# Optimization experiments

Hardware: AMD Instinct MI355X
Metric: run time of the kernel (lower is better)

The kernel has to match this reference:

```python
import jax, jax.numpy as jnp
import numpy as np

B, D, H = 4096, 1024, 1024

def _glorot(key, shape):
    fan_in, fan_out = shape
    limit = np.sqrt(6.0 / (fan_in + fan_out))
    return jax.random.uniform(key, shape, jnp.float32, -limit, limit)

def setup_inputs() -> dict:
    key = jax.random.key(0)
    ks = jax.random.split(key, 12)
    inp = {
        'inputs': jax.random.normal(ks[0], (B, D), jnp.float32),
        'h_prev': jax.random.normal(ks[1], (B, H), jnp.float32),
        'c_prev': jax.random.normal(ks[2], (B, H), jnp.float32),
    }
    names = ['f', 'i', 'c', 'o']
    for j, n in enumerate(names):
        inp['W_' + n] = _glorot(ks[3 + 2 * j], (D, H))
        inp['U_' + n] = _glorot(ks[4 + 2 * j], (H, H))
        inp['b_' + n] = jnp.zeros((H,), jnp.float32)
    return inp

def reference(inputs, h_prev, c_prev, W_f, U_f, b_f, W_i, U_i, b_i, W_c, U_c, b_c, W_o, U_o, b_o):
    f_t = jax.nn.sigmoid(inputs @ W_f + h_prev @ U_f + b_f)
    i_t = jax.nn.sigmoid(inputs @ W_i + h_prev @ U_i + b_i)
    c_tilde = jnp.tanh(inputs @ W_c + h_prev @ U_c + b_c)
    c_next = f_t * c_prev + i_t * c_tilde
    o_t = jax.nn.sigmoid(inputs @ W_o + h_prev @ U_o + b_o)
    h_next = o_t * jnp.tanh(c_next)
    return (h_next, c_next)
```

## Files before the change

kernel.cpp:

```cpp
#include <hip/hip_runtime.h>


typedef __attribute__((ext_vector_type(8))) short bfrag8;
typedef __attribute__((ext_vector_type(4))) float f32x4;

__device__ __forceinline__ unsigned int f2bf(float f) {
  unsigned int u = __builtin_bit_cast(unsigned int, f);
  unsigned int r = (u + 0x7fffu + ((u >> 16) & 1u)) >> 16;
  return r & 0xffffu;
}

__global__ __launch_bounds__(256) void prep_x(const float* __restrict__ inputs,
                                              const float* __restrict__ h_prev,
                                              unsigned short* __restrict__ X) {
  int idx = blockIdx.x * 256 + threadIdx.x;
  int b  = idx >> 8;
  int k8 = (idx & 255) * 8;
  const float* src = (k8 < 1024) ? (inputs + (size_t)b * 1024 + k8)
                                 : (h_prev + (size_t)b * 1024 + (k8 - 1024));
  float4 v0 = ((const float4*)src)[0];
  float4 v1 = ((const float4*)src)[1];
  uint4 o;
  o.x = f2bf(v0.x) | (f2bf(v0.y) << 16);
  o.y = f2bf(v0.z) | (f2bf(v0.w) << 16);
  o.z = f2bf(v1.x) | (f2bf(v1.y) << 16);
  o.w = f2bf(v1.z) | (f2bf(v1.w) << 16);
  *(uint4*)(X + (size_t)b * 2048 + k8) = o;
}

__global__ __launch_bounds__(256) void prep_w(
    const float* __restrict__ s0, const float* __restrict__ s1,
    const float* __restrict__ s2, const float* __restrict__ s3,
    const float* __restrict__ s4, const float* __restrict__ s5,
    const float* __restrict__ s6, const float* __restrict__ s7,
    unsigned short* __restrict__ Wct) {
  int blk = blockIdx.x;
  int m = blk >> 8;
  const float* src = (m == 0) ? s0 : (m == 1) ? s1 : (m == 2) ? s2 : (m == 3) ? s3
                   : (m == 4) ? s4 : (m == 5) ? s5 : (m == 6) ? s6 : s7;
  int g = m >> 1, half = m & 1;
  unsigned short* dst = Wct + (size_t)g * 1024 * 2048 + (size_t)half * 1024;
  int t = blk & 255;
  int k0 = (t >> 4) * 64;
  int h0 = (t & 15) * 64;
  __shared__ float lt[64][68];
  int tid = threadIdx.x;
  #pragma unroll
  for (int it = 0; it < 4; ++it) {
    int r  = (tid >> 4) + it * 16;
    int c4 = (tid & 15) * 4;
    float4 v = *(const float4*)(src + (size_t)(k0 + r) * 1024 + h0 + c4);
    lt[r][c4 + 0] = v.x; lt[r][c4 + 1] = v.y; lt[r][c4 + 2] = v.z; lt[r][c4 + 3] = v.w;
  }
  __syncthreads();
  #pragma unroll
  for (int it = 0; it < 4; ++it) {
    int hh  = (tid >> 4) + it * 16;
    int kk4 = (tid & 15) * 4;
    uint2 o;
    o.x = f2bf(lt[kk4 + 0][hh]) | (f2bf(lt[kk4 + 1][hh]) << 16);
    o.y = f2bf(lt[kk4 + 2][hh]) | (f2bf(lt[kk4 + 3][hh]) << 16);
    *(uint2*)(dst + (size_t)(h0 + hh) * 2048 + k0 + kk4) = o;
  }
}

__global__ __launch_bounds__(256, 2) void lstm_gemm(
    const unsigned short* __restrict__ X, const unsigned short* __restrict__ Wct,
    const float* __restrict__ c_prev,
    const float* __restrict__ bfv, const float* __restrict__ biv,
    const float* __restrict__ bcv, const float* __restrict__ bov,
    float* __restrict__ out) {
  __shared__ __align__(16) char smem[49152];
  const int tid = threadIdx.x;
  const int lane = tid & 63, wid = tid >> 6;
  const int u = lane & 15, q = lane >> 4;
  const int wave_m = wid >> 1, wave_n = wid & 1;
  const int h0 = blockIdx.x * 64;
  const int row0 = blockIdx.y * 128;

  f32x4 acc[4][4][2];
  #pragma unroll
  for (int g = 0; g < 4; ++g)
    #pragma unroll
    for (int mi = 0; mi < 4; ++mi)
      #pragma unroll
      for (int ni = 0; ni < 2; ++ni)
        acc[g][mi][ni] = (f32x4){0.f, 0.f, 0.f, 0.f};

  #pragma unroll 1
  for (int kt = 0; kt < 32; ++kt) {
    const int kb = kt * 64;
    __syncthreads();
    #pragma unroll
    for (int i = 0; i < 4; ++i) {
      int c = tid + 256 * i;
      int row = c >> 3, slot = c & 7;
      int sw = slot ^ (row & 7);
      uint4 v = *(const uint4*)(X + (size_t)(row0 + row) * 2048 + kb + slot * 8);
      *(uint4*)(smem + row * 128 + sw * 16) = v;
    }
    #pragma unroll
    for (int i = 0; i < 8; ++i) {
      int c = tid + 256 * i;
      int g = c >> 9, hr = (c >> 3) & 63, slot = c & 7;
      int sw = slot ^ (hr & 7);
      uint4 v = *(const uint4*)(Wct + (size_t)((g << 10) + h0 + hr) * 2048 + kb + slot * 8);
      *(uint4*)(smem + 16384 + g * 8192 + hr * 128 + sw * 16) = v;
    }
    __syncthreads();
    #pragma unroll
    for (int kk = 0; kk < 2; ++kk) {
      bfrag8 afr[4];
      #pragma unroll
      for (int mi = 0; mi < 4; ++mi) {
        int row = wave_m * 64 + mi * 16 + u;
        int sl = (kk * 4 + q) ^ (row & 7);
        afr[mi] = *(const bfrag8*)(smem + row * 128 + sl * 16);
      }
      #pragma unroll
      for (int g = 0; g < 4; ++g) {
        #pragma unroll
        for (int ni = 0; ni < 2; ++ni) {
          int hr = wave_n * 32 + ni * 16 + u;
          int sl = (kk * 4 + q) ^ (hr & 7);
          bfrag8 bfr = *(const bfrag8*)(smem + 16384 + g * 8192 + hr * 128 + sl * 16);
          #pragma unroll
          for (int mi = 0; mi < 4; ++mi)
            acc[g][mi][ni] = __builtin_amdgcn_mfma_f32_16x16x32_bf16(
                afr[mi], bfr, acc[g][mi][ni], 0, 0, 0);
        }
      }
    }
  }

  #pragma unroll
  for (int ni = 0; ni < 2; ++ni) {
    int h = h0 + wave_n * 32 + ni * 16 + u;
    float Bf = bfv[h], Bi = biv[h], Bc = bcv[h], Bo = bov[h];
    #pragma unroll
    for (int mi = 0; mi < 4; ++mi) {
      #pragma unroll
      for (int j = 0; j < 4; ++j) {
        int b = row0 + wave_m * 64 + mi * 16 + q * 4 + j;
        float pf = acc[0][mi][ni][j] + Bf;
        float pi = acc[1][mi][ni][j] + Bi;
        float pc = acc[2][mi][ni][j] + Bc;
        float po = acc[3][mi][ni][j] + Bo;
        float fg = 1.f / (1.f + __expf(-pf));
        float ig = 1.f / (1.f + __expf(-pi));
        float ct = 2.f / (1.f + __expf(-2.f * pc)) - 1.f;
        float og = 1.f / (1.f + __expf(-po));
        float cn = fg * c_prev[(size_t)b * 1024 + h] + ig * ct;
        float hn = og * (2.f / (1.f + __expf(-2.f * cn)) - 1.f);
        out[(size_t)b * 1024 + h] = hn;
        out[(size_t)4096 * 1024 + (size_t)b * 1024 + h] = cn;
      }
    }
  }
}

extern "C" void kernel_launch(void* const* d_in, const int* in_sizes, int n_in,
                              void* d_out, int out_size, void* d_ws, size_t ws_size,
                              hipStream_t stream) {
  const float* inputs = (const float*)d_in[0];
  const float* h_prev = (const float*)d_in[1];
  const float* c_prev = (const float*)d_in[2];
  const float* Wf = (const float*)d_in[3];
  const float* Uf = (const float*)d_in[4];
  const float* bf = (const float*)d_in[5];
  const float* Wi = (const float*)d_in[6];
  const float* Ui = (const float*)d_in[7];
  const float* bi = (const float*)d_in[8];
  const float* Wc = (const float*)d_in[9];
  const float* Uc = (const float*)d_in[10];
  const float* bc = (const float*)d_in[11];
  const float* Wo = (const float*)d_in[12];
  const float* Uo = (const float*)d_in[13];
  const float* bo = (const float*)d_in[14];
  float* out = (float*)d_out;

  unsigned short* X   = (unsigned short*)d_ws;
  unsigned short* Wct = X + (size_t)4096 * 2048;

  prep_x<<<4096, 256, 0, stream>>>(inputs, h_prev, X);
  prep_w<<<2048, 256, 0, stream>>>(Wf, Uf, Wi, Ui, Wc, Uc, Wo, Uo, Wct);
  dim3 grid(16, 32);
  lstm_gemm<<<grid, 256, 0, stream>>>(X, Wct, c_prev, bf, bi, bc, bo, out);
}
```

Measured before the change: 95.61 us.

## Rewrite LSTM GEMM as 256x256-tile, 8-wave, double-buffered direct-to-LDS pipeline

Replaces the 128x64-tile GEMM with a 256-row by 64-hidden (times 4 gates) tile per 512-thread block, using 128KB of dynamic LDS. Global data is staged straight into LDS with global_load_lds, double-buffered over k and interleaved with ds_read and MFMA phases, with explicit vmcnt and lgkmcnt waits, barriers, and setprio around MFMA bursts. A block-ID swizzle is added for L2 locality. The aim is to hide global-load latency and raise reuse per LDS byte, at the cost of a much more fragile, hand-scheduled pipeline and only 256 blocks.

```diff
diff --git a/kernel.cpp b/kernel.cpp
--- a/kernel.cpp
+++ b/kernel.cpp
@@ -64,97 +64,183 @@
   }
 }
 
-__global__ __launch_bounds__(256, 2) void lstm_gemm(
+
+#define FENCE() asm volatile("" ::: "memory")
+#define BARRIER() do { FENCE(); __builtin_amdgcn_s_barrier(); FENCE(); } while (0)
+#define VMCNT(n) asm volatile("s_waitcnt vmcnt(" #n ")" ::: "memory")
+#define LGKM0_SCHED() do { asm volatile("s_waitcnt lgkmcnt(0)" ::: "memory"); \
+                           __builtin_amdgcn_sched_barrier(0); } while (0)
+#define GLOAD16(gp, lp) __builtin_amdgcn_global_load_lds( \
+    (const __attribute__((address_space(1))) unsigned int*)(gp), \
+    (__attribute__((address_space(3))) unsigned int*)(lp), 16, 0, 0)
+#define DSR(dst, addr, off) asm volatile("ds_read_b128 %0, %1 offset:%c2" \
+    : "=v"(dst) : "v"(addr), "n"(off))
+
+#define READ_A8(arr, BUF, RB) do { \
+  DSR(arr[0], aA0, (BUF)*16384 + (RB)*128 + 0);    \
+  DSR(arr[1], aA1, (BUF)*16384 + (RB)*128 + 0);    \
+  DSR(arr[2], aA0, (BUF)*16384 + (RB)*128 + 2048); \
+  DSR(arr[3], aA1, (BUF)*16384 + (RB)*128 + 2048); \
+  DSR(arr[4], aA0, (BUF)*16384 + (RB)*128 + 4096); \
+  DSR(arr[5], aA1, (BUF)*16384 + (RB)*128 + 4096); \
+  DSR(arr[6], aA0, (BUF)*16384 + (RB)*128 + 6144); \
+  DSR(arr[7], aA1, (BUF)*16384 + (RB)*128 + 6144); \
+} while (0)
+
+#define READ_B4(arr, BUF, CB) do { \
+  DSR(arr[0], aB0, (BUF)*16384 + (CB)*128 + 0);    \
+  DSR(arr[1], aB1, (BUF)*16384 + (CB)*128 + 0);    \
+  DSR(arr[2], aB0, (BUF)*16384 + (CB)*128 + 2048); \
+  DSR(arr[3], aB1, (BUF)*16384 + (CB)*128 + 2048); \
+} while (0)
+
+#define STAGE_A(BUF, H, kt) do { int _kb = ((kt) < 32 ? (kt) : 31) * 64; \
+  GLOAD16(pA0 + (size_t)(H) * 262144 + _kb, smem + (H)*32768 + (BUF)*16384 + stbase); \
+  GLOAD16(pA1 + (size_t)(H) * 262144 + _kb, smem + (H)*32768 + (BUF)*16384 + stbase + 1024); \
+} while (0)
+
+#define STAGE_B0(BUF, kt) do { int _kb = ((kt) < 32 ? (kt) : 31) * 64; \
+  GLOAD16(pB00 + _kb, smem + 65536 + (BUF)*16384 + stbase); \
+  GLOAD16(pB01 + _kb, smem + 65536 + (BUF)*16384 + stbase + 1024); \
+} while (0)
+
+#define STAGE_B1(BUF, kt) do { int _kb = ((kt) < 32 ? (kt) : 31) * 64; \
+  GLOAD16(pB10 + _kb, smem + 98304 + (BUF)*16384 + stbase); \
+  GLOAD16(pB11 + _kb, smem + 98304 + (BUF)*16384 + stbase + 1024); \
+} while (0)
+
+#define MFMA16(B4, G0, M0) do { \
+  __builtin_amdgcn_s_setprio(1); \
+  _Pragma("unroll") for (int ni = 0; ni < 2; ++ni) \
+  _Pragma("unroll") for (int mi = 0; mi < 4; ++mi) \
+  _Pragma("unroll") for (int kk = 0; kk < 2; ++kk) \
+    acc[(G0)+ni][(M0)+mi] = __builtin_amdgcn_mfma_f32_16x16x32_bf16( \
+        a[mi*2+kk], (B4)[ni*2+kk], acc[(G0)+ni][(M0)+mi], 0, 0, 0); \
+  __builtin_amdgcn_s_setprio(0); \
+} while (0)
+
+__global__ __launch_bounds__(512, 2) void lstm_gemm(
     const unsigned short* __restrict__ X, const unsigned short* __restrict__ Wct,
     const float* __restrict__ c_prev,
     const float* __restrict__ bfv, const float* __restrict__ biv,
     const float* __restrict__ bcv, const float* __restrict__ bov,
     float* __restrict__ out) {
-  __shared__ __align__(16) char smem[49152];
+  extern __shared__ __align__(16) char smem[];
   const int tid = threadIdx.x;
-  const int lane = tid & 63, wid = tid >> 6;
-  const int u = lane & 15, q = lane >> 4;
-  const int wave_m = wid >> 1, wave_n = wid & 1;
-  const int h0 = blockIdx.x * 64;
-  const int row0 = blockIdx.y * 128;
-
-  f32x4 acc[4][4][2];
+  const int lane = tid & 63, w = tid >> 6;
+  const int u = lane & 15, q = (lane >> 4) & 3;
+  const int wm = w >> 2, wn = w & 3;
+
+  const int bid = blockIdx.x;
+  const int swz = (bid & 7) * 32 + (bid >> 3);
+  const int h0 = (swz & 15) * 64;
+  const int row0 = (swz >> 4) * 256;
+
+  const unsigned lds0 = (unsigned)(size_t)((__attribute__((address_space(3))) char*)smem);
+
+  const int sw0 = (q ^ (u & 7)) << 4;
+  const int sw1 = ((q + 4) ^ (u & 7)) << 4;
+  const unsigned aA0 = lds0 + wm * 32768 + u * 128 + sw0;
+  const unsigned aA1 = lds0 + wm * 32768 + u * 128 + sw1;
+  const unsigned aB0 = lds0 + 65536 + (wn >> 1) * 32768 + ((wn & 1) * 64 + u) * 128 + sw0;
+  const unsigned aB1 = lds0 + 65536 + (wn >> 1) * 32768 + ((wn & 1) * 64 + u) * 128 + sw1;
+
+  const int stbase = w * 2048 + lane * 16;
+  const int rA0 = w * 16 + (lane >> 3), rA1 = rA0 + 8;
+  const int ssA = (lane & 7) ^ (rA0 & 7);
+  const unsigned short* pA0 = X + (size_t)(row0 + rA0) * 2048 + ssA * 8;
+  const unsigned short* pA1 = X + (size_t)(row0 + rA1) * 2048 + ssA * 8;
+  auto wrow = [&](int C) { return (((C >> 4) & 3) << 10) + h0 + ((C >> 6) << 4) + (C & 15); };
+  const unsigned short* pB00 = Wct + (size_t)wrow(rA0) * 2048 + ssA * 8;
+  const unsigned short* pB01 = Wct + (size_t)wrow(rA1) * 2048 + ssA * 8;
+  const unsigned short* pB10 = Wct + (size_t)wrow(128 + rA0) * 2048 + ssA * 8;
+  const unsigned short* pB11 = Wct + (size_t)wrow(128 + rA1) * 2048 + ssA * 8;
+
+  f32x4 acc[4][8];
   #pragma unroll
   for (int g = 0; g < 4; ++g)
     #pragma unroll
-    for (int mi = 0; mi < 4; ++mi)
-      #pragma unroll
-      for (int ni = 0; ni < 2; ++ni)
-        acc[g][mi][ni] = (f32x4){0.f, 0.f, 0.f, 0.f};
+    for (int m = 0; m < 8; ++m)
+      acc[g][m] = (f32x4){0.f, 0.f, 0.f, 0.f};
+
+  bfrag8 a[8], bh[4], bl0[4], bl1[4];
+
+  STAGE_B0(0, 0); STAGE_B1(0, 0); STAGE_A(0, 0, 0); STAGE_A(0, 1, 0);
+  STAGE_B0(1, 1); STAGE_B1(1, 1);
+  VMCNT(4);
+  BARRIER();
+  READ_B4(bl0, 0, 0);
 
   #pragma unroll 1
-  for (int kt = 0; kt < 32; ++kt) {
-    const int kb = kt * 64;
-    __syncthreads();
+  for (int t = 0; t < 16; ++t) {
+    const int kt1 = 2 * t + 1, kt2 = 2 * t + 2, kt3 = 2 * t + 3;
+    READ_A8(a, 0, 0);
+    STAGE_A(1, 0, kt1);
+    BARRIER(); LGKM0_SCHED();
+    MFMA16(bl0, 0, 0);
+    BARRIER();
+    READ_B4(bh, 0, 32);
+    STAGE_A(1, 1, kt1);
+    BARRIER(); LGKM0_SCHED();
+    MFMA16(bh, 2, 0);
+    BARRIER();
+    READ_A8(a, 0, 64);
+    STAGE_B0(0, kt2);
+    VMCNT(8);
+    BARRIER(); LGKM0_SCHED();
+    MFMA16(bh, 2, 4);
+    BARRIER();
+    READ_B4(bl1, 1, 0);
+    STAGE_B1(0, kt2);
+    VMCNT(4);
+    BARRIER(); LGKM0_SCHED();
+    MFMA16(bl0, 0, 4);
+    BARRIER();
+    READ_A8(a, 1, 0);
+    STAGE_A(0, 0, kt2);
+    BARRIER(); LGKM0_SCHED();
+    MFMA16(bl1, 0, 0);
+    BARRIER();
+    READ_B4(bh, 1, 32);
+    STAGE_A(0, 1, kt2);
+    BARRIER(); LGKM0_SCHED();
+    MFMA16(bh, 2, 0);
+    BARRIER();
+    READ_A8(a, 1, 64);
+    STAGE_B0(1, kt3);
+    VMCNT(8);
+    BARRIER(); LGKM0_SCHED();
+    MFMA16(bh, 2, 4);
+    BARRIER();
+    READ_B4(bl0, 0, 0);
+    STAGE_B1(1, kt3);
+    VMCNT(4);
+    BARRIER(); LGKM0_SCHED();
+    MFMA16(bl1, 0, 4);
+    BARRIER();
+  }
+  VMCNT(0);
+
+  const int hcol = h0 + wn * 16 + u;
+  const float Bgf = bfv[hcol], Bgi = biv[hcol], Bgc = bcv[hcol], Bgo = bov[hcol];
+  const int rbw = row0 + wm * 128;
+  #pragma unroll
+  for (int m = 0; m < 8; ++m) {
     #pragma unroll
-    for (int i = 0; i < 4; ++i) {
-      int c = tid + 256 * i;
-      int row = c >> 3, slot = c & 7;
-      int sw = slot ^ (row & 7);
-      uint4 v = *(const uint4*)(X + (size_t)(row0 + row) * 2048 + kb + slot * 8);
-      *(uint4*)(smem + row * 128 + sw * 16) = v;
-    }
-    #pragma unroll
-    for (int i = 0; i < 8; ++i) {
-      int c = tid + 256 * i;
-      int g = c >> 9, hr = (c >> 3) & 63, slot = c & 7;
-      int sw = slot ^ (hr & 7);
-      uint4 v = *(const uint4*)(Wct + (size_t)((g << 10) + h0 + hr) * 2048 + kb + slot * 8);
-      *(uint4*)(smem + 16384 + g * 8192 + hr * 128 + sw * 16) = v;
-    }
-    __syncthreads();
-    #pragma unroll
-    for (int kk = 0; kk < 2; ++kk) {
-      bfrag8 afr[4];
-      #pragma unroll
-      for (int mi = 0; mi < 4; ++mi) {
-        int row = wave_m * 64 + mi * 16 + u;
-        int sl = (kk * 4 + q) ^ (row & 7);
-        afr[mi] = *(const bfrag8*)(smem + row * 128 + sl * 16);
-      }
-      #pragma unroll
-      for (int g = 0; g < 4; ++g) {
-        #pragma unroll
-        for (int ni = 0; ni < 2; ++ni) {
-          int hr = wave_n * 32 + ni * 16 + u;
-          int sl = (kk * 4 + q) ^ (hr & 7);
-          bfrag8 bfr = *(const bfrag8*)(smem + 16384 + g * 8192 + hr * 128 + sl * 16);
-          #pragma unroll
-          for (int mi = 0; mi < 4; ++mi)
-            acc[g][mi][ni] = __builtin_amdgcn_mfma_f32_16x16x32_bf16(
-                afr[mi], bfr, acc[g][mi][ni], 0, 0, 0);
-        }
-      }
-    }
-  }
-
-  #pragma unroll
-  for (int ni = 0; ni < 2; ++ni) {
-    int h = h0 + wave_n * 32 + ni * 16 + u;
-    float Bf = bfv[h], Bi = biv[h], Bc = bcv[h], Bo = bov[h];
-    #pragma unroll
-    for (int mi = 0; mi < 4; ++mi) {
-      #pragma unroll
-      for (int j = 0; j < 4; ++j) {
-        int b = row0 + wave_m * 64 + mi * 16 + q * 4 + j;
-        float pf = acc[0][mi][ni][j] + Bf;
-        float pi = acc[1][mi][ni][j] + Bi;
-        float pc = acc[2][mi][ni][j] + Bc;
-        float po = acc[3][mi][ni][j] + Bo;
-        float fg = 1.f / (1.f + __expf(-pf));
-        float ig = 1.f / (1.f + __expf(-pi));
-        float ct = 2.f / (1.f + __expf(-2.f * pc)) - 1.f;
-        float og = 1.f / (1.f + __expf(-po));
-        float cn = fg * c_prev[(size_t)b * 1024 + h] + ig * ct;
-        float hn = og * (2.f / (1.f + __expf(-2.f * cn)) - 1.f);
-        out[(size_t)b * 1024 + h] = hn;
-        out[(size_t)4096 * 1024 + (size_t)b * 1024 + h] = cn;
-      }
+    for (int j = 0; j < 4; ++j) {
+      const int b = rbw + m * 16 + q * 4 + j;
+      float pf = acc[0][m][j] + Bgf;
+      float pi = acc[1][m][j] + Bgi;
+      float pc = acc[2][m][j] + Bgc;
+      float po = acc[3][m][j] + Bgo;
+      float fg = 1.f / (1.f + __expf(-pf));
+      float ig = 1.f / (1.f + __expf(-pi));
+      float ct = 2.f / (1.f + __expf(-2.f * pc)) - 1.f;
+      float og = 1.f / (1.f + __expf(-po));
+      float cn = fg * c_prev[(size_t)b * 1024 + hcol] + ig * ct;
+      float hn = og * (2.f / (1.f + __expf(-2.f * cn)) - 1.f);
+      out[(size_t)b * 1024 + hcol] = hn;
+      out[(size_t)4096 * 1024 + (size_t)b * 1024 + hcol] = cn;
     }
   }
 }
@@ -182,8 +268,10 @@
   unsigned short* X   = (unsigned short*)d_ws;
   unsigned short* Wct = X + (size_t)4096 * 2048;
 
+  (void)hipFuncSetAttribute(reinterpret_cast<const void*>(lstm_gemm),
+                            hipFuncAttributeMaxDynamicSharedMemorySize, 131072);
+
   prep_x<<<4096, 256, 0, stream>>>(inputs, h_prev, X);
   prep_w<<<2048, 256, 0, stream>>>(Wf, Uf, Wi, Ui, Wc, Uc, Wo, Uo, Wct);
-  dim3 grid(16, 32);
-  lstm_gemm<<<grid, 256, 0, stream>>>(X, Wct, c_prev, bf, bi, bc, bo, out);
-}
+  lstm_gemm<<<256, 512, 131072, stream>>>(X, Wct, c_prev, bf, bi, bc, bo, out);
+}
```

Measured after the change: 88.73 us. -7.2%, faster.
